# Optimization experiments

Measured on AMD Instinct MI355X. Metric: run time of the kernel, lower is better.

## Reference

```python
import jax, jax.numpy as jnp
import numpy as np

C = 256
CQK = C // 8  # 32

def setup_inputs() -> dict:
    key = jax.random.key(0)
    ks = jax.random.split(key, 9)
    B, H, W = 4, 64, 64
    shp = (B, C, H, W)
    v = jax.random.normal(ks[0], shp, dtype=jnp.float32)
    k = jax.random.normal(ks[1], shp, dtype=jnp.float32)
    q = jax.random.normal(ks[2], shp, dtype=jnp.float32)
    s = 1.0 / np.sqrt(C)
    Wq = jax.random.normal(ks[3], (CQK, C), dtype=jnp.float32) * s
    bq = jnp.zeros((CQK,), dtype=jnp.float32)
    Wk = jax.random.normal(ks[4], (CQK, C), dtype=jnp.float32) * s
    bk = jnp.zeros((CQK,), dtype=jnp.float32)
    Wv = jax.random.normal(ks[5], (C, C), dtype=jnp.float32) * s
    bv = jnp.zeros((C,), dtype=jnp.float32)
    # torch inits gamma=0 (out == v); use small nonzero so attention path is exercised
    gamma = jnp.full((1,), 0.5, dtype=jnp.float32)
    return {"v": v, "k": k, "q": q, "Wq": Wq, "bq": bq, "Wk": Wk, "bk": bk,
            "Wv": Wv, "bv": bv, "gamma": gamma}

def reference(v, k, q, Wq, bq, Wk, bk, Wv, bv, gamma):
    B, Cc, Hh, Ww = v.shape
    N = Hh * Ww
    # 1x1 convs == per-pixel channel matmuls
    pq = jnp.einsum('oc,bchw->bohw', Wq, q) + bq[None, :, None, None]  # B,CQK,H,W
    pk = jnp.einsum('oc,bchw->bohw', Wk, k) + bk[None, :, None, None]
    pv = jnp.einsum('oc,bchw->bohw', Wv, v) + bv[None, :, None, None]  # B,C,H,W
    pq = pq.reshape(B, -1, N)  # B,d,N
    pk = pk.reshape(B, -1, N)
    pv = pv.reshape(B, Cc, N)
    # energy[b,n,m] = <q_n, k_m>; softmax over m (keys)
    energy = jnp.einsum('bdn,bdm->bnm', pq, pk)
    attn = jax.nn.softmax(energy, axis=-1)
    # out[b,c,n] = sum_m v[b,c,m] * attn[b,n,m]
    out = jnp.einsum('bcm,bnm->bcn', pv, attn).reshape(B, Cc, Hh, Ww)
    return gamma * out + v
```

## Files before the change

### kernel.cpp

```cpp
#include <hip/hip_runtime.h>
#include <hip/hip_bf16.h>

typedef __attribute__((ext_vector_type(8))) short short8_t;
typedef __attribute__((ext_vector_type(4))) short short4_t;
typedef __attribute__((ext_vector_type(4))) float float4_t;

#define B_   4
#define C_   256
#define N_   4096
#define DQK  32
#define LOG2E 1.4426950408889634f

#define VMCNT4   asm volatile("s_waitcnt vmcnt(4)" ::: "memory")
#define LGKM0    asm volatile("s_waitcnt lgkmcnt(0)" ::: "memory")
#define SBAR     __builtin_amdgcn_s_barrier()
#define SCHEDB   __builtin_amdgcn_sched_barrier(0)

__device__ __forceinline__ unsigned short f2bf(float x) {
    union { float f; unsigned int u; } v; v.f = x;
    unsigned int r = v.u + 0x7FFFu + ((v.u >> 16) & 1u);
    return (unsigned short)(r >> 16);
}
__device__ __forceinline__ unsigned short f2bf_hw(float x) {
    return __bfloat16_as_ushort(__float2bfloat16(x));
}

__global__ __launch_bounds__(256) void cast_w_k(
        const float* __restrict__ Wq, const float* __restrict__ Wk,
        const float* __restrict__ Wv,
        unsigned short* __restrict__ Wqb, unsigned short* __restrict__ Wkb,
        unsigned short* __restrict__ Wvb) {
    int i = blockIdx.x * 256 + threadIdx.x;
    if (i < 8192)            Wqb[i] = f2bf(Wq[i]);
    else if (i < 16384)      Wkb[i - 8192] = f2bf(Wk[i - 8192]);
    else                     Wvb[i - 16384] = f2bf(Wv[i - 16384]);
}

__global__ __launch_bounds__(256) void proj_qk_k(
        const float* __restrict__ q_in, const float* __restrict__ k_in,
        const unsigned short* __restrict__ Wqb, const unsigned short* __restrict__ Wkb,
        const float* __restrict__ bq, const float* __restrict__ bk,
        unsigned short* __restrict__ pqT, unsigned short* __restrict__ pkT) {
    int b = blockIdx.y, z = blockIdx.z;
    const float* X = z ? k_in : q_in;
    const unsigned short* W = z ? Wkb : Wqb;
    const float* bias = z ? bk : bq;
    unsigned short* P = z ? pkT : pqT;
    float scl = z ? 1.0f : LOG2E;
    int tid = threadIdx.x, wave = tid >> 6, lane = tid & 63, l15 = lane & 15, g = lane >> 4;
    int nb = blockIdx.x * 64 + wave * 16;
    float4_t acc0 = {0.f, 0.f, 0.f, 0.f}, acc1 = {0.f, 0.f, 0.f, 0.f};
    const float* Xcol = X + (size_t)b * C_ * N_ + nb + l15;
#pragma unroll
    for (int kk = 0; kk < 8; ++kk) {
        short8_t a;
#pragma unroll
        for (int j = 0; j < 8; ++j)
            a[j] = (short)f2bf(Xcol[(size_t)(kk * 32 + 8 * g + j) * N_]);
        short8_t b0 = *(const short8_t*)(W + (size_t)l15 * C_ + kk * 32 + 8 * g);
        short8_t b1 = *(const short8_t*)(W + (size_t)(16 + l15) * C_ + kk * 32 + 8 * g);
        acc0 = __builtin_amdgcn_mfma_f32_16x16x32_bf16(a, b0, acc0, 0, 0, 0);
        acc1 = __builtin_amdgcn_mfma_f32_16x16x32_bf16(a, b1, acc1, 0, 0, 0);
    }
#pragma unroll
    for (int r = 0; r < 4; ++r) {
        int n = nb + 4 * g + r;
        P[((size_t)b * N_ + n) * DQK + l15]      = f2bf((acc0[r] + bias[l15]) * scl);
        P[((size_t)b * N_ + n) * DQK + 16 + l15] = f2bf((acc1[r] + bias[16 + l15]) * scl);
    }
}

__global__ __launch_bounds__(256) void proj_v_k(
        const float* __restrict__ v_in, const unsigned short* __restrict__ Wvb,
        const float* __restrict__ bv, unsigned short* __restrict__ pv) {
    int b = blockIdx.y;
    int tid = threadIdx.x, wave = tid >> 6, lane = tid & 63, l15 = lane & 15, g = lane >> 4;
    int mb = blockIdx.x * 16;
    int m = mb + l15;
    int k32 = m & 31;
    int pcol = (k32 < 16) ? ((k32 >> 2) * 8 + (k32 & 3))
                          : (((k32 - 16) >> 2) * 8 + 4 + (k32 & 3));
    int mcol = (m & ~31) + pcol;
    float4_t acc[4];
#pragma unroll
    for (int i = 0; i < 4; ++i) acc[i] = (float4_t){0.f, 0.f, 0.f, 0.f};
    const float* Vcol = v_in + (size_t)b * C_ * N_ + mb + l15;
#pragma unroll
    for (int kk = 0; kk < 8; ++kk) {
        short8_t bf;
#pragma unroll
        for (int j = 0; j < 8; ++j)
            bf[j] = (short)f2bf(Vcol[(size_t)(kk * 32 + 8 * g + j) * N_]);
#pragma unroll
        for (int ct = 0; ct < 4; ++ct) {
            short8_t af = *(const short8_t*)(Wvb + (size_t)(wave * 64 + ct * 16 + l15) * C_ + kk * 32 + 8 * g);
            acc[ct] = __builtin_amdgcn_mfma_f32_16x16x32_bf16(af, bf, acc[ct], 0, 0, 0);
        }
    }
#pragma unroll
    for (int ct = 0; ct < 4; ++ct)
#pragma unroll
        for (int r = 0; r < 4; ++r) {
            int c = wave * 64 + ct * 16 + 4 * g + r;
            pv[((size_t)b * C_ + c) * N_ + mcol] = f2bf(acc[ct][r] + bv[c]);
        }
}

__global__ __launch_bounds__(256, 2) void attn_split_k(
        const unsigned short* __restrict__ pqT, const unsigned short* __restrict__ pkT,
        const unsigned short* __restrict__ pv,
        float* __restrict__ accP, float* __restrict__ lP, int KS) {
    __shared__ __align__(16) unsigned short VT[2][256][64];
    int nqb = gridDim.x;
    int lin = blockIdx.x + nqb * (blockIdx.y + KS * blockIdx.z);
    int cpx = (nqb * KS * 4) >> 3;
    int sl  = (lin & 7) * cpx + (lin >> 3);
    int qbi = sl % nqb;
    int s   = (sl / nqb) % KS;
    int b   = sl / (nqb * KS);

    int kps = N_ / KS, ks0 = s * kps, nt = kps >> 6;
    int tid = threadIdx.x, wave = tid >> 6, lane = tid & 63, l15 = lane & 15, g = lane >> 4;
    int qb = qbi * 64;
    int sw = (l15 & 7) << 4;
    int rl = lane >> 3, cp = lane & 7, cl = cp ^ rl;

    short8_t qf = *(const short8_t*)(pqT + ((size_t)b * N_ + qb + wave * 16 + l15) * DQK + 8 * g);
    float4_t acc[16];
#pragma unroll
    for (int i = 0; i < 16; ++i) acc[i] = (float4_t){0.f, 0.f, 0.f, 0.f};
    float l_acc = 0.f;
    const float4_t zero4 = {0.f, 0.f, 0.f, 0.f};
    const unsigned short* pvb = pv + (size_t)b * C_ * N_;

#define LOADG(dst, base)                                                      \
    _Pragma("unroll")                                                         \
    for (int i_ = 0; i_ < 4; ++i_) {                                          \
        const char* vrow_ = vb + (((base) + i_) * 16 + l15) * 128;            \
        dst[i_][0] = *(const short8_t*)(vrow_ + ((16 * g) ^ sw));             \
        dst[i_][1] = *(const short8_t*)(vrow_ + ((64 + 16 * g) ^ sw));        \
    }
#define MFMAG(frag, ctbase)                                                   \
    _Pragma("unroll")                                                         \
    for (int i_ = 0; i_ < 4; ++i_) {                                          \
        acc[(ctbase) + i_] = __builtin_amdgcn_mfma_f32_16x16x32_bf16(frag[i_][0], pb0, acc[(ctbase) + i_], 0, 0, 0); \
        acc[(ctbase) + i_] = __builtin_amdgcn_mfma_f32_16x16x32_bf16(frag[i_][1], pb1, acc[(ctbase) + i_], 0, 0, 0); \
    }

#pragma unroll
    for (int i = 0; i < 8; ++i) {
        int row0 = wave * 64 + i * 8;
        const unsigned short* src = pvb + (size_t)(row0 + rl) * N_ + ks0 + 8 * cl;
        __builtin_amdgcn_global_load_lds(
            (const __attribute__((address_space(1))) unsigned int*)(const void*)src,
            (__attribute__((address_space(3))) unsigned int*)(void*)&VT[0][row0][0], 16, 0, 0);
    }
    short8_t kfc[4];
#pragma unroll
    for (int it = 0; it < 4; ++it)
        kfc[it] = *(const short8_t*)(pkT + ((size_t)b * N_ + ks0 + 16 * it + l15) * DQK + 8 * g);
    VMCNT4; SCHEDB;
    SBAR;

    for (int t = 0; t < nt; ++t) {
        const int rb = t & 1;
        const int msn = ks0 + (t + 1) * 64;
        if (t + 1 < nt) {
#pragma unroll
            for (int i = 0; i < 8; ++i) {
                int row0 = wave * 64 + i * 8;
                const unsigned short* src = pvb + (size_t)(row0 + rl) * N_ + msn + 8 * cl;
                __builtin_amdgcn_global_load_lds(
                    (const __attribute__((address_space(1))) unsigned int*)(const void*)src,
                    (__attribute__((address_space(3))) unsigned int*)(void*)&VT[rb ^ 1][row0][0], 16, 0, 0);
            }
        }
        SCHEDB;
        const char* vb = (const char*)&VT[rb][0][0];
        short8_t vg0[4][2], vg1[4][2];
        LOADG(vg0, 0);
        LOADG(vg1, 4);
        float4_t sv[4];
#pragma unroll
        for (int it = 0; it < 4; ++it)
            sv[it] = __builtin_amdgcn_mfma_f32_16x16x32_bf16(kfc[it], qf, zero4, 0, 0, 0);
        short8_t kfn[4];
        if (t + 1 < nt) {
#pragma unroll
            for (int it = 0; it < 4; ++it)
                kfn[it] = *(const short8_t*)(pkT + ((size_t)b * N_ + msn + 16 * it + l15) * DQK + 8 * g);
        }
        float p[16];
#pragma unroll
        for (int it = 0; it < 4; ++it)
#pragma unroll
            for (int r = 0; r < 4; ++r)
                p[it * 4 + r] = exp2f(sv[it][r]);
        float s0 = (p[0] + p[1]) + (p[2] + p[3]);
        float s1 = (p[4] + p[5]) + (p[6] + p[7]);
        float s2 = (p[8] + p[9]) + (p[10] + p[11]);
        float s3 = (p[12] + p[13]) + (p[14] + p[15]);
        l_acc += (s0 + s1) + (s2 + s3);
        short8_t pb0, pb1;
#pragma unroll
        for (int j = 0; j < 4; ++j) {
            pb0[j]     = (short)f2bf_hw(p[j]);
            pb0[4 + j] = (short)f2bf_hw(p[4 + j]);
            pb1[j]     = (short)f2bf_hw(p[8 + j]);
            pb1[4 + j] = (short)f2bf_hw(p[12 + j]);
        }
        __builtin_amdgcn_s_setprio(1);
        MFMAG(vg0, 0);
        LOADG(vg0, 8);
        MFMAG(vg1, 4);
        LOADG(vg1, 12);
        MFMAG(vg0, 8);
        MFMAG(vg1, 12);
        __builtin_amdgcn_s_setprio(0);
        if (t + 1 < nt) {
            LGKM0; SCHEDB;
            SBAR;
            VMCNT4; SCHEDB;
            SBAR;
#pragma unroll
            for (int it = 0; it < 4; ++it) kfc[it] = kfn[it];
        }
    }

    l_acc += __shfl_xor(l_acc, 16);
    l_acc += __shfl_xor(l_acc, 32);
    if (g == 0)
        lP[(size_t)(b * KS + s) * N_ + qb + wave * 16 + l15] = l_acc;
    float* accOut = accP + ((size_t)(b * KS + s) * C_) * N_;
#pragma unroll
    for (int ct = 0; ct < 16; ++ct)
#pragma unroll
        for (int r = 0; r < 4; ++r) {
            int c = ct * 16 + 4 * g + r;
            accOut[(size_t)c * N_ + qb + wave * 16 + l15] = acc[ct][r];
        }
#undef LOADG
#undef MFMAG
}

__global__ __launch_bounds__(256) void combine_k(
        const float* __restrict__ accP, const float* __restrict__ lP,
        const float* __restrict__ v_in, const float* __restrict__ gamma,
        float* __restrict__ out, int KS) {
    int i = blockIdx.x * 256 + threadIdx.x;
    const int nq4 = N_ / 4;
    int q0 = (i % nq4) * 4;
    int c  = (i / nq4) % C_;
    int b  = i / (nq4 * C_);
    float4_t num = {0.f, 0.f, 0.f, 0.f}, den = {0.f, 0.f, 0.f, 0.f};
    for (int s = 0; s < KS; ++s) {
        float4_t l4 = *(const float4_t*)(lP + (size_t)(b * KS + s) * N_ + q0);
        float4_t a4 = *(const float4_t*)(accP + ((size_t)(b * KS + s) * C_ + c) * N_ + q0);
#pragma unroll
        for (int j = 0; j < 4; ++j) {
            den[j] += l4[j];
            num[j] += a4[j];
        }
    }
    float gm = gamma[0];
    size_t idx = ((size_t)(b * C_ + c)) * N_ + q0;
    float4_t vi = *(const float4_t*)(v_in + idx);
    float4_t o;
#pragma unroll
    for (int j = 0; j < 4; ++j) o[j] = gm * num[j] / den[j] + vi[j];
    *(float4_t*)(out + idx) = o;
}

extern "C" void kernel_launch(void* const* d_in, const int* in_sizes, int n_in,
                              void* d_out, int out_size, void* d_ws, size_t ws_size,
                              hipStream_t stream) {
    (void)in_sizes; (void)n_in; (void)out_size;
    const float* v_in  = (const float*)d_in[0];
    const float* k_in  = (const float*)d_in[1];
    const float* q_in  = (const float*)d_in[2];
    const float* Wq    = (const float*)d_in[3];
    const float* bq    = (const float*)d_in[4];
    const float* Wk    = (const float*)d_in[5];
    const float* bk    = (const float*)d_in[6];
    const float* Wv    = (const float*)d_in[7];
    const float* bv    = (const float*)d_in[8];
    const float* gamma = (const float*)d_in[9];
    float* out = (float*)d_out;

    char* ws = (char*)d_ws;
    unsigned short* pvb = (unsigned short*)(ws + 0);
    unsigned short* pqT = (unsigned short*)(ws + 8388608);
    unsigned short* pkT = (unsigned short*)(ws + 9437184);
    unsigned short* Wqb = (unsigned short*)(ws + 10485760);
    unsigned short* Wkb = (unsigned short*)(ws + 10502144);
    unsigned short* Wvb = (unsigned short*)(ws + 10518528);
    const size_t base2 = 10649600;

    int KS = 2;
    while (KS > 1) {
        size_t need = base2 + (size_t)KS * 16777216 + (size_t)KS * 262144;
        if (need <= ws_size) break;
        KS >>= 1;
    }
    float* accP = (float*)(ws + base2);
    float* lP   = (float*)(ws + base2 + (size_t)KS * 16777216);

    cast_w_k<<<320, 256, 0, stream>>>(Wq, Wk, Wv, Wqb, Wkb, Wvb);
    proj_qk_k<<<dim3(64, 4, 2), 256, 0, stream>>>(q_in, k_in, Wqb, Wkb, bq, bk, pqT, pkT);
    proj_v_k<<<dim3(256, 4), 256, 0, stream>>>(v_in, Wvb, bv, pvb);
    attn_split_k<<<dim3(64, KS, 4), 256, 0, stream>>>(pqT, pkT, pvb, accP, lP, KS);
    combine_k<<<4096, 256, 0, stream>>>(accP, lP, v_in, gamma, out, KS);
}
```

Baseline: 102.3 us.

## Fuse combine into attention kernel and drop split-K with 8-wave channel split

```diff
diff --git a/kernel.cpp b/kernel.cpp
--- a/kernel.cpp
+++ b/kernel.cpp
@@ -106,37 +106,31 @@
         }
 }
 
-__global__ __launch_bounds__(256, 2) void attn_split_k(
+__global__ __launch_bounds__(512, 2) void attn_fused_k(
         const unsigned short* __restrict__ pqT, const unsigned short* __restrict__ pkT,
-        const unsigned short* __restrict__ pv,
-        float* __restrict__ accP, float* __restrict__ lP, int KS) {
+        const unsigned short* __restrict__ pv, const float* __restrict__ v_in,
+        const float* __restrict__ gamma, float* __restrict__ out) {
     __shared__ __align__(16) unsigned short VT[2][256][64];
-    int nqb = gridDim.x;
-    int lin = blockIdx.x + nqb * (blockIdx.y + KS * blockIdx.z);
-    int cpx = (nqb * KS * 4) >> 3;
-    int sl  = (lin & 7) * cpx + (lin >> 3);
-    int qbi = sl % nqb;
-    int s   = (sl / nqb) % KS;
-    int b   = sl / (nqb * KS);
-
-    int kps = N_ / KS, ks0 = s * kps, nt = kps >> 6;
+    int b = blockIdx.z;
+    int qb = blockIdx.x * 64;
     int tid = threadIdx.x, wave = tid >> 6, lane = tid & 63, l15 = lane & 15, g = lane >> 4;
-    int qb = qbi * 64;
+    int wq = wave & 3, wc = wave >> 2;
     int sw = (l15 & 7) << 4;
     int rl = lane >> 3, cp = lane & 7, cl = cp ^ rl;
-
-    short8_t qf = *(const short8_t*)(pqT + ((size_t)b * N_ + qb + wave * 16 + l15) * DQK + 8 * g);
-    float4_t acc[16];
-#pragma unroll
-    for (int i = 0; i < 16; ++i) acc[i] = (float4_t){0.f, 0.f, 0.f, 0.f};
+    const int nt = N_ / 64;
+
+    short8_t qf = *(const short8_t*)(pqT + ((size_t)b * N_ + qb + wq * 16 + l15) * DQK + 8 * g);
+    float4_t acc[8];
+#pragma unroll
+    for (int i = 0; i < 8; ++i) acc[i] = (float4_t){0.f, 0.f, 0.f, 0.f};
     float l_acc = 0.f;
     const float4_t zero4 = {0.f, 0.f, 0.f, 0.f};
     const unsigned short* pvb = pv + (size_t)b * C_ * N_;
 
-#define LOADG(dst, base)                                                      \
+#define LOADG(dst, ctbase)                                                    \
     _Pragma("unroll")                                                         \
     for (int i_ = 0; i_ < 4; ++i_) {                                          \
-        const char* vrow_ = vb + (((base) + i_) * 16 + l15) * 128;            \
+        const char* vrow_ = vb + (((ctbase) + i_) * 16 + l15) * 128;          \
         dst[i_][0] = *(const short8_t*)(vrow_ + ((16 * g) ^ sw));             \
         dst[i_][1] = *(const short8_t*)(vrow_ + ((64 + 16 * g) ^ sw));        \
     }
@@ -148,9 +142,9 @@
     }
 
 #pragma unroll
-    for (int i = 0; i < 8; ++i) {
-        int row0 = wave * 64 + i * 8;
-        const unsigned short* src = pvb + (size_t)(row0 + rl) * N_ + ks0 + 8 * cl;
+    for (int i = 0; i < 4; ++i) {
+        int row0 = i * 64 + wave * 8;
+        const unsigned short* src = pvb + (size_t)(row0 + rl) * N_ + 8 * cl;
         __builtin_amdgcn_global_load_lds(
             (const __attribute__((address_space(1))) unsigned int*)(const void*)src,
             (__attribute__((address_space(3))) unsigned int*)(void*)&VT[0][row0][0], 16, 0, 0);
@@ -158,17 +152,17 @@
     short8_t kfc[4];
 #pragma unroll
     for (int it = 0; it < 4; ++it)
-        kfc[it] = *(const short8_t*)(pkT + ((size_t)b * N_ + ks0 + 16 * it + l15) * DQK + 8 * g);
+        kfc[it] = *(const short8_t*)(pkT + ((size_t)b * N_ + 16 * it + l15) * DQK + 8 * g);
     VMCNT4; SCHEDB;
     SBAR;
 
     for (int t = 0; t < nt; ++t) {
         const int rb = t & 1;
-        const int msn = ks0 + (t + 1) * 64;
+        const int msn = (t + 1) * 64;
         if (t + 1 < nt) {
 #pragma unroll
-            for (int i = 0; i < 8; ++i) {
-                int row0 = wave * 64 + i * 8;
+            for (int i = 0; i < 4; ++i) {
+                int row0 = i * 64 + wave * 8;
                 const unsigned short* src = pvb + (size_t)(row0 + rl) * N_ + msn + 8 * cl;
                 __builtin_amdgcn_global_load_lds(
                     (const __attribute__((address_space(1))) unsigned int*)(const void*)src,
@@ -176,7 +170,7 @@
             }
         }
         SCHEDB;
-        const char* vb = (const char*)&VT[rb][0][0];
+        const char* vb = (const char*)&VT[rb][0][0] + wc * 16384;
         short8_t vg0[4][2], vg1[4][2];
         LOADG(vg0, 0);
         LOADG(vg1, 4);
@@ -211,11 +205,7 @@
         }
         __builtin_amdgcn_s_setprio(1);
         MFMAG(vg0, 0);
-        LOADG(vg0, 8);
         MFMAG(vg1, 4);
-        LOADG(vg1, 12);
-        MFMAG(vg0, 8);
-        MFMAG(vg1, 12);
         __builtin_amdgcn_s_setprio(0);
         if (t + 1 < nt) {
             LGKM0; SCHEDB;
@@ -229,52 +219,24 @@
 
     l_acc += __shfl_xor(l_acc, 16);
     l_acc += __shfl_xor(l_acc, 32);
-    if (g == 0)
-        lP[(size_t)(b * KS + s) * N_ + qb + wave * 16 + l15] = l_acc;
-    float* accOut = accP + ((size_t)(b * KS + s) * C_) * N_;
-#pragma unroll
-    for (int ct = 0; ct < 16; ++ct)
+    float inv = 1.f / l_acc;
+    float gm = gamma[0];
+#pragma unroll
+    for (int ct = 0; ct < 8; ++ct)
 #pragma unroll
         for (int r = 0; r < 4; ++r) {
-            int c = ct * 16 + 4 * g + r;
-            accOut[(size_t)c * N_ + qb + wave * 16 + l15] = acc[ct][r];
+            int c = wc * 128 + ct * 16 + 4 * g + r;
+            size_t idx = ((size_t)(b * C_ + c)) * N_ + qb + wq * 16 + l15;
+            out[idx] = gm * acc[ct][r] * inv + v_in[idx];
         }
 #undef LOADG
 #undef MFMAG
-}
-
-__global__ __launch_bounds__(256) void combine_k(
-        const float* __restrict__ accP, const float* __restrict__ lP,
-        const float* __restrict__ v_in, const float* __restrict__ gamma,
-        float* __restrict__ out, int KS) {
-    int i = blockIdx.x * 256 + threadIdx.x;
-    const int nq4 = N_ / 4;
-    int q0 = (i % nq4) * 4;
-    int c  = (i / nq4) % C_;
-    int b  = i / (nq4 * C_);
-    float4_t num = {0.f, 0.f, 0.f, 0.f}, den = {0.f, 0.f, 0.f, 0.f};
-    for (int s = 0; s < KS; ++s) {
-        float4_t l4 = *(const float4_t*)(lP + (size_t)(b * KS + s) * N_ + q0);
-        float4_t a4 = *(const float4_t*)(accP + ((size_t)(b * KS + s) * C_ + c) * N_ + q0);
-#pragma unroll
-        for (int j = 0; j < 4; ++j) {
-            den[j] += l4[j];
-            num[j] += a4[j];
-        }
-    }
-    float gm = gamma[0];
-    size_t idx = ((size_t)(b * C_ + c)) * N_ + q0;
-    float4_t vi = *(const float4_t*)(v_in + idx);
-    float4_t o;
-#pragma unroll
-    for (int j = 0; j < 4; ++j) o[j] = gm * num[j] / den[j] + vi[j];
-    *(float4_t*)(out + idx) = o;
 }
 
 extern "C" void kernel_launch(void* const* d_in, const int* in_sizes, int n_in,
                               void* d_out, int out_size, void* d_ws, size_t ws_size,
                               hipStream_t stream) {
-    (void)in_sizes; (void)n_in; (void)out_size;
+    (void)in_sizes; (void)n_in; (void)out_size; (void)ws_size;
     const float* v_in  = (const float*)d_in[0];
     const float* k_in  = (const float*)d_in[1];
     const float* q_in  = (const float*)d_in[2];
@@ -294,20 +256,9 @@
     unsigned short* Wqb = (unsigned short*)(ws + 10485760);
     unsigned short* Wkb = (unsigned short*)(ws + 10502144);
     unsigned short* Wvb = (unsigned short*)(ws + 10518528);
-    const size_t base2 = 10649600;
-
-    int KS = 2;
-    while (KS > 1) {
-        size_t need = base2 + (size_t)KS * 16777216 + (size_t)KS * 262144;
-        if (need <= ws_size) break;
-        KS >>= 1;
-    }
-    float* accP = (float*)(ws + base2);
-    float* lP   = (float*)(ws + base2 + (size_t)KS * 16777216);
 
     cast_w_k<<<320, 256, 0, stream>>>(Wq, Wk, Wv, Wqb, Wkb, Wvb);
     proj_qk_k<<<dim3(64, 4, 2), 256, 0, stream>>>(q_in, k_in, Wqb, Wkb, bq, bk, pqT, pkT);
     proj_v_k<<<dim3(256, 4), 256, 0, stream>>>(v_in, Wvb, bv, pvb);
-    attn_split_k<<<dim3(64, KS, 4), 256, 0, stream>>>(pqT, pkT, pvb, accP, lP, KS);
-    combine_k<<<4096, 256, 0, stream>>>(accP, lP, v_in, gamma, out, KS);
-}
+    attn_fused_k<<<dim3(64, 1, 4), 512, 0, stream>>>(pqT, pkT, pvb, v_in, gamma, out);
+}
```

Result: slower. 123.1 us (+20.3%).

## Retile split-K attention waves into 2x2 query/channel grid with MFMA row sums

Applied to the files above, without the earlier changes.

```diff
diff --git a/kernel.cpp b/kernel.cpp
--- a/kernel.cpp
+++ b/kernel.cpp
@@ -121,31 +121,28 @@
 
     int kps = N_ / KS, ks0 = s * kps, nt = kps >> 6;
     int tid = threadIdx.x, wave = tid >> 6, lane = tid & 63, l15 = lane & 15, g = lane >> 4;
+    int wq = wave & 1, wc = wave >> 1;
     int qb = qbi * 64;
     int sw = (l15 & 7) << 4;
     int rl = lane >> 3, cp = lane & 7, cl = cp ^ rl;
 
-    short8_t qf = *(const short8_t*)(pqT + ((size_t)b * N_ + qb + wave * 16 + l15) * DQK + 8 * g);
-    float4_t acc[16];
-#pragma unroll
-    for (int i = 0; i < 16; ++i) acc[i] = (float4_t){0.f, 0.f, 0.f, 0.f};
-    float l_acc = 0.f;
+    short8_t qf[2];
+#pragma unroll
+    for (int qs = 0; qs < 2; ++qs)
+        qf[qs] = *(const short8_t*)(pqT + ((size_t)b * N_ + qb + wq * 32 + qs * 16 + l15) * DQK + 8 * g);
+    float4_t acc[2][8];
+#pragma unroll
+    for (int qs = 0; qs < 2; ++qs)
+#pragma unroll
+        for (int i = 0; i < 8; ++i) acc[qs][i] = (float4_t){0.f, 0.f, 0.f, 0.f};
+    float4_t accl[2];
+    accl[0] = (float4_t){0.f, 0.f, 0.f, 0.f};
+    accl[1] = (float4_t){0.f, 0.f, 0.f, 0.f};
+    short8_t onef;
+#pragma unroll
+    for (int j = 0; j < 8; ++j) onef[j] = (short)0x3F80;
     const float4_t zero4 = {0.f, 0.f, 0.f, 0.f};
     const unsigned short* pvb = pv + (size_t)b * C_ * N_;
-
-#define LOADG(dst, base)                                                      \
-    _Pragma("unroll")                                                         \
-    for (int i_ = 0; i_ < 4; ++i_) {                                          \
-        const char* vrow_ = vb + (((base) + i_) * 16 + l15) * 128;            \
-        dst[i_][0] = *(const short8_t*)(vrow_ + ((16 * g) ^ sw));             \
-        dst[i_][1] = *(const short8_t*)(vrow_ + ((64 + 16 * g) ^ sw));        \
-    }
-#define MFMAG(frag, ctbase)                                                   \
-    _Pragma("unroll")                                                         \
-    for (int i_ = 0; i_ < 4; ++i_) {                                          \
-        acc[(ctbase) + i_] = __builtin_amdgcn_mfma_f32_16x16x32_bf16(frag[i_][0], pb0, acc[(ctbase) + i_], 0, 0, 0); \
-        acc[(ctbase) + i_] = __builtin_amdgcn_mfma_f32_16x16x32_bf16(frag[i_][1], pb1, acc[(ctbase) + i_], 0, 0, 0); \
-    }
 
 #pragma unroll
     for (int i = 0; i < 8; ++i) {
@@ -176,46 +173,51 @@
             }
         }
         SCHEDB;
-        const char* vb = (const char*)&VT[rb][0][0];
-        short8_t vg0[4][2], vg1[4][2];
-        LOADG(vg0, 0);
-        LOADG(vg1, 4);
-        float4_t sv[4];
-#pragma unroll
-        for (int it = 0; it < 4; ++it)
-            sv[it] = __builtin_amdgcn_mfma_f32_16x16x32_bf16(kfc[it], qf, zero4, 0, 0, 0);
+        float4_t sv[2][4];
+#pragma unroll
+        for (int qs = 0; qs < 2; ++qs)
+#pragma unroll
+            for (int it = 0; it < 4; ++it)
+                sv[qs][it] = __builtin_amdgcn_mfma_f32_16x16x32_bf16(kfc[it], qf[qs], zero4, 0, 0, 0);
         short8_t kfn[4];
         if (t + 1 < nt) {
 #pragma unroll
             for (int it = 0; it < 4; ++it)
                 kfn[it] = *(const short8_t*)(pkT + ((size_t)b * N_ + msn + 16 * it + l15) * DQK + 8 * g);
         }
-        float p[16];
-#pragma unroll
-        for (int it = 0; it < 4; ++it)
-#pragma unroll
-            for (int r = 0; r < 4; ++r)
-                p[it * 4 + r] = exp2f(sv[it][r]);
-        float s0 = (p[0] + p[1]) + (p[2] + p[3]);
-        float s1 = (p[4] + p[5]) + (p[6] + p[7]);
-        float s2 = (p[8] + p[9]) + (p[10] + p[11]);
-        float s3 = (p[12] + p[13]) + (p[14] + p[15]);
-        l_acc += (s0 + s1) + (s2 + s3);
-        short8_t pb0, pb1;
-#pragma unroll
-        for (int j = 0; j < 4; ++j) {
-            pb0[j]     = (short)f2bf_hw(p[j]);
-            pb0[4 + j] = (short)f2bf_hw(p[4 + j]);
-            pb1[j]     = (short)f2bf_hw(p[8 + j]);
-            pb1[4 + j] = (short)f2bf_hw(p[12 + j]);
-        }
+        short8_t pb[2][2];
+#pragma unroll
+        for (int qs = 0; qs < 2; ++qs) {
+            float p[16];
+#pragma unroll
+            for (int it = 0; it < 4; ++it)
+#pragma unroll
+                for (int r = 0; r < 4; ++r)
+                    p[it * 4 + r] = exp2f(sv[qs][it][r]);
+#pragma unroll
+            for (int j = 0; j < 4; ++j) {
+                pb[qs][0][j]     = (short)f2bf_hw(p[j]);
+                pb[qs][0][4 + j] = (short)f2bf_hw(p[4 + j]);
+                pb[qs][1][j]     = (short)f2bf_hw(p[8 + j]);
+                pb[qs][1][4 + j] = (short)f2bf_hw(p[12 + j]);
+            }
+        }
+        const char* vb = (const char*)&VT[rb][0][0] + wc * 16384;
         __builtin_amdgcn_s_setprio(1);
-        MFMAG(vg0, 0);
-        LOADG(vg0, 8);
-        MFMAG(vg1, 4);
-        LOADG(vg1, 12);
-        MFMAG(vg0, 8);
-        MFMAG(vg1, 12);
+#pragma unroll
+        for (int ct = 0; ct < 8; ++ct) {
+            const char* vrow = vb + (ct * 16 + l15) * 128;
+            short8_t va0 = *(const short8_t*)(vrow + ((16 * g) ^ sw));
+            short8_t va1 = *(const short8_t*)(vrow + ((64 + 16 * g) ^ sw));
+            acc[0][ct] = __builtin_amdgcn_mfma_f32_16x16x32_bf16(va0, pb[0][0], acc[0][ct], 0, 0, 0);
+            acc[0][ct] = __builtin_amdgcn_mfma_f32_16x16x32_bf16(va1, pb[0][1], acc[0][ct], 0, 0, 0);
+            acc[1][ct] = __builtin_amdgcn_mfma_f32_16x16x32_bf16(va0, pb[1][0], acc[1][ct], 0, 0, 0);
+            acc[1][ct] = __builtin_amdgcn_mfma_f32_16x16x32_bf16(va1, pb[1][1], acc[1][ct], 0, 0, 0);
+        }
+        accl[0] = __builtin_amdgcn_mfma_f32_16x16x32_bf16(onef, pb[0][0], accl[0], 0, 0, 0);
+        accl[0] = __builtin_amdgcn_mfma_f32_16x16x32_bf16(onef, pb[0][1], accl[0], 0, 0, 0);
+        accl[1] = __builtin_amdgcn_mfma_f32_16x16x32_bf16(onef, pb[1][0], accl[1], 0, 0, 0);
+        accl[1] = __builtin_amdgcn_mfma_f32_16x16x32_bf16(onef, pb[1][1], accl[1], 0, 0, 0);
         __builtin_amdgcn_s_setprio(0);
         if (t + 1 < nt) {
             LGKM0; SCHEDB;
@@ -227,20 +229,20 @@
         }
     }
 
-    l_acc += __shfl_xor(l_acc, 16);
-    l_acc += __shfl_xor(l_acc, 32);
-    if (g == 0)
-        lP[(size_t)(b * KS + s) * N_ + qb + wave * 16 + l15] = l_acc;
     float* accOut = accP + ((size_t)(b * KS + s) * C_) * N_;
 #pragma unroll
-    for (int ct = 0; ct < 16; ++ct)
-#pragma unroll
-        for (int r = 0; r < 4; ++r) {
-            int c = ct * 16 + 4 * g + r;
-            accOut[(size_t)c * N_ + qb + wave * 16 + l15] = acc[ct][r];
-        }
-#undef LOADG
-#undef MFMAG
+    for (int qs = 0; qs < 2; ++qs) {
+        int q = qb + wq * 32 + qs * 16 + l15;
+#pragma unroll
+        for (int ct = 0; ct < 8; ++ct)
+#pragma unroll
+            for (int r = 0; r < 4; ++r) {
+                int c = wc * 128 + ct * 16 + 4 * g + r;
+                accOut[(size_t)c * N_ + q] = acc[qs][ct][r];
+            }
+        if (wc == 0 && g == 0)
+            lP[(size_t)(b * KS + s) * N_ + q] = accl[qs][0];
+    }
 }
 
 __global__ __launch_bounds__(256) void combine_k(
```

After: 112.3 us. +9.7%, slower.

## Software-pipeline QK/exp one tile ahead and compute row sums via MFMA

Applied to the files above, without the earlier changes.

```diff
diff --git a/kernel.cpp b/kernel.cpp
--- a/kernel.cpp
+++ b/kernel.cpp
@@ -12,6 +12,7 @@
 #define LOG2E 1.4426950408889634f
 
 #define VMCNT4   asm volatile("s_waitcnt vmcnt(4)" ::: "memory")
+#define VMCNT0   asm volatile("s_waitcnt vmcnt(0)" ::: "memory")
 #define LGKM0    asm volatile("s_waitcnt lgkmcnt(0)" ::: "memory")
 #define SBAR     __builtin_amdgcn_s_barrier()
 #define SCHEDB   __builtin_amdgcn_sched_barrier(0)
@@ -123,114 +124,107 @@
     int tid = threadIdx.x, wave = tid >> 6, lane = tid & 63, l15 = lane & 15, g = lane >> 4;
     int qb = qbi * 64;
     int sw = (l15 & 7) << 4;
-    int rl = lane >> 3, cp = lane & 7, cl = cp ^ rl;
+    int rl = lane >> 3, cl = (lane & 7) ^ rl;
 
     short8_t qf = *(const short8_t*)(pqT + ((size_t)b * N_ + qb + wave * 16 + l15) * DQK + 8 * g);
     float4_t acc[16];
 #pragma unroll
     for (int i = 0; i < 16; ++i) acc[i] = (float4_t){0.f, 0.f, 0.f, 0.f};
-    float l_acc = 0.f;
+    float4_t accl = {0.f, 0.f, 0.f, 0.f};
+    short8_t onef;
+#pragma unroll
+    for (int j = 0; j < 8; ++j) onef[j] = (short)0x3F80;
     const float4_t zero4 = {0.f, 0.f, 0.f, 0.f};
     const unsigned short* pvb = pv + (size_t)b * C_ * N_;
-
-#define LOADG(dst, base)                                                      \
+    const char* pkTb = (const char*)pkT + (size_t)b * N_ * DQK * 2;
+
+    unsigned soff[8];
+#pragma unroll
+    for (int i = 0; i < 8; ++i)
+        soff[i] = (unsigned)(((wave * 64 + i * 8 + rl) * N_ + ks0 + 8 * cl) * 2);
+    unsigned koff = (unsigned)(((ks0 + l15) * DQK + 8 * g) * 2);
+    int off1 = (16 * g) ^ sw, off2 = (64 + 16 * g) ^ sw;
+    const char* vbA = (const char*)&VT[0][0][0] + l15 * 128 + off1;
+    const char* vbB = (const char*)&VT[0][0][0] + l15 * 128 + off2;
+
+#define STAGE(RBUF)                                                           \
     _Pragma("unroll")                                                         \
-    for (int i_ = 0; i_ < 4; ++i_) {                                          \
-        const char* vrow_ = vb + (((base) + i_) * 16 + l15) * 128;            \
-        dst[i_][0] = *(const short8_t*)(vrow_ + ((16 * g) ^ sw));             \
-        dst[i_][1] = *(const short8_t*)(vrow_ + ((64 + 16 * g) ^ sw));        \
-    }
-#define MFMAG(frag, ctbase)                                                   \
+    for (int i_ = 0; i_ < 8; ++i_) {                                          \
+        __builtin_amdgcn_global_load_lds(                                     \
+            (const __attribute__((address_space(1))) unsigned int*)(const void*)((const char*)pvb + soff[i_]), \
+            (__attribute__((address_space(3))) unsigned int*)(void*)&VT[RBUF][wave * 64 + i_ * 8][0], 16, 0, 0); \
+    }                                                                          \
     _Pragma("unroll")                                                         \
-    for (int i_ = 0; i_ < 4; ++i_) {                                          \
-        acc[(ctbase) + i_] = __builtin_amdgcn_mfma_f32_16x16x32_bf16(frag[i_][0], pb0, acc[(ctbase) + i_], 0, 0, 0); \
-        acc[(ctbase) + i_] = __builtin_amdgcn_mfma_f32_16x16x32_bf16(frag[i_][1], pb1, acc[(ctbase) + i_], 0, 0, 0); \
-    }
-
-#pragma unroll
-    for (int i = 0; i < 8; ++i) {
-        int row0 = wave * 64 + i * 8;
-        const unsigned short* src = pvb + (size_t)(row0 + rl) * N_ + ks0 + 8 * cl;
-        __builtin_amdgcn_global_load_lds(
-            (const __attribute__((address_space(1))) unsigned int*)(const void*)src,
-            (__attribute__((address_space(3))) unsigned int*)(void*)&VT[0][row0][0], 16, 0, 0);
-    }
-    short8_t kfc[4];
-#pragma unroll
-    for (int it = 0; it < 4; ++it)
-        kfc[it] = *(const short8_t*)(pkT + ((size_t)b * N_ + ks0 + 16 * it + l15) * DQK + 8 * g);
-    VMCNT4; SCHEDB;
+    for (int i_ = 0; i_ < 8; ++i_) soff[i_] += 128;
+
+#define KFLOAD(DST)                                                           \
+    _Pragma("unroll")                                                         \
+    for (int it_ = 0; it_ < 4; ++it_)                                         \
+        DST[it_] = *(const short8_t*)(pkTb + koff + it_ * 1024);              \
+    koff += 4096;
+
+#define QKEXP(KF, PN0, PN1)                                                   \
+    {                                                                          \
+        float4_t sv_[4];                                                       \
+        _Pragma("unroll")                                                      \
+        for (int it_ = 0; it_ < 4; ++it_)                                      \
+            sv_[it_] = __builtin_amdgcn_mfma_f32_16x16x32_bf16(KF[it_], qf, zero4, 0, 0, 0); \
+        float p_[16];                                                          \
+        _Pragma("unroll")                                                      \
+        for (int it_ = 0; it_ < 4; ++it_)                                      \
+            _Pragma("unroll")                                                  \
+            for (int r_ = 0; r_ < 4; ++r_)                                     \
+                p_[it_ * 4 + r_] = exp2f(sv_[it_][r_]);                        \
+        _Pragma("unroll")                                                      \
+        for (int j_ = 0; j_ < 4; ++j_) {                                       \
+            PN0[j_]     = (short)f2bf_hw(p_[j_]);                              \
+            PN0[4 + j_] = (short)f2bf_hw(p_[4 + j_]);                          \
+            PN1[j_]     = (short)f2bf_hw(p_[8 + j_]);                          \
+            PN1[4 + j_] = (short)f2bf_hw(p_[12 + j_]);                         \
+        }                                                                      \
+    }
+
+#define PVPH(RB, PC0, PC1)                                                    \
+    __builtin_amdgcn_s_setprio(1);                                            \
+    _Pragma("unroll")                                                         \
+    for (int ct_ = 0; ct_ < 16; ++ct_) {                                      \
+        short8_t va0_ = *(const short8_t*)(vbA + (RB) * 32768 + ct_ * 2048);  \
+        short8_t va1_ = *(const short8_t*)(vbB + (RB) * 32768 + ct_ * 2048);  \
+        acc[ct_] = __builtin_amdgcn_mfma_f32_16x16x32_bf16(va0_, PC0, acc[ct_], 0, 0, 0); \
+        acc[ct_] = __builtin_amdgcn_mfma_f32_16x16x32_bf16(va1_, PC1, acc[ct_], 0, 0, 0); \
+    }                                                                          \
+    accl = __builtin_amdgcn_mfma_f32_16x16x32_bf16(onef, PC0, accl, 0, 0, 0); \
+    accl = __builtin_amdgcn_mfma_f32_16x16x32_bf16(onef, PC1, accl, 0, 0, 0); \
+    __builtin_amdgcn_s_setprio(0);
+
+#define BODY(RB, KFC, KFN, PC0, PC1, PN0, PN1, TT)                            \
+    if ((TT) + 1 < nt) { STAGE(RB ^ 1) }                                      \
+    SCHEDB;                                                                   \
+    KFLOAD(KFN)                                                               \
+    QKEXP(KFC, PN0, PN1)                                                      \
+    PVPH(RB, PC0, PC1)                                                        \
+    LGKM0; SCHEDB;                                                            \
+    SBAR;                                                                     \
+    VMCNT4; SCHEDB;                                                           \
     SBAR;
 
-    for (int t = 0; t < nt; ++t) {
-        const int rb = t & 1;
-        const int msn = ks0 + (t + 1) * 64;
-        if (t + 1 < nt) {
-#pragma unroll
-            for (int i = 0; i < 8; ++i) {
-                int row0 = wave * 64 + i * 8;
-                const unsigned short* src = pvb + (size_t)(row0 + rl) * N_ + msn + 8 * cl;
-                __builtin_amdgcn_global_load_lds(
-                    (const __attribute__((address_space(1))) unsigned int*)(const void*)src,
-                    (__attribute__((address_space(3))) unsigned int*)(void*)&VT[rb ^ 1][row0][0], 16, 0, 0);
-            }
-        }
-        SCHEDB;
-        const char* vb = (const char*)&VT[rb][0][0];
-        short8_t vg0[4][2], vg1[4][2];
-        LOADG(vg0, 0);
-        LOADG(vg1, 4);
-        float4_t sv[4];
-#pragma unroll
-        for (int it = 0; it < 4; ++it)
-            sv[it] = __builtin_amdgcn_mfma_f32_16x16x32_bf16(kfc[it], qf, zero4, 0, 0, 0);
-        short8_t kfn[4];
-        if (t + 1 < nt) {
-#pragma unroll
-            for (int it = 0; it < 4; ++it)
-                kfn[it] = *(const short8_t*)(pkT + ((size_t)b * N_ + msn + 16 * it + l15) * DQK + 8 * g);
-        }
-        float p[16];
-#pragma unroll
-        for (int it = 0; it < 4; ++it)
-#pragma unroll
-            for (int r = 0; r < 4; ++r)
-                p[it * 4 + r] = exp2f(sv[it][r]);
-        float s0 = (p[0] + p[1]) + (p[2] + p[3]);
-        float s1 = (p[4] + p[5]) + (p[6] + p[7]);
-        float s2 = (p[8] + p[9]) + (p[10] + p[11]);
-        float s3 = (p[12] + p[13]) + (p[14] + p[15]);
-        l_acc += (s0 + s1) + (s2 + s3);
-        short8_t pb0, pb1;
-#pragma unroll
-        for (int j = 0; j < 4; ++j) {
-            pb0[j]     = (short)f2bf_hw(p[j]);
-            pb0[4 + j] = (short)f2bf_hw(p[4 + j]);
-            pb1[j]     = (short)f2bf_hw(p[8 + j]);
-            pb1[4 + j] = (short)f2bf_hw(p[12 + j]);
-        }
-        __builtin_amdgcn_s_setprio(1);
-        MFMAG(vg0, 0);
-        LOADG(vg0, 8);
-        MFMAG(vg1, 4);
-        LOADG(vg1, 12);
-        MFMAG(vg0, 8);
-        MFMAG(vg1, 12);
-        __builtin_amdgcn_s_setprio(0);
-        if (t + 1 < nt) {
-            LGKM0; SCHEDB;
-            SBAR;
-            VMCNT4; SCHEDB;
-            SBAR;
-#pragma unroll
-            for (int it = 0; it < 4; ++it) kfc[it] = kfn[it];
-        }
-    }
-
-    l_acc += __shfl_xor(l_acc, 16);
-    l_acc += __shfl_xor(l_acc, 32);
+    short8_t kfA[4], kfB[4];
+    short8_t pbA0, pbA1, pbB0, pbB1;
+    STAGE(0)
+    SCHEDB;
+    KFLOAD(kfB)
+    KFLOAD(kfA)
+    VMCNT0; SCHEDB;
+    QKEXP(kfB, pbB0, pbB1)
+    SBAR;
+
+    for (int t = 0; t < nt; t += 2) {
+        BODY(0, kfA, kfB, pbB0, pbB1, pbA0, pbA1, t)
+        BODY(1, kfB, kfA, pbA0, pbA1, pbB0, pbB1, t + 1)
+    }
+
     if (g == 0)
-        lP[(size_t)(b * KS + s) * N_ + qb + wave * 16 + l15] = l_acc;
+        lP[(size_t)(b * KS + s) * N_ + qb + wave * 16 + l15] = accl[0];
     float* accOut = accP + ((size_t)(b * KS + s) * C_) * N_;
 #pragma unroll
     for (int ct = 0; ct < 16; ++ct)
@@ -239,8 +233,11 @@
             int c = ct * 16 + 4 * g + r;
             accOut[(size_t)c * N_ + qb + wave * 16 + l15] = acc[ct][r];
         }
-#undef LOADG
-#undef MFMAG
+#undef STAGE
+#undef KFLOAD
+#undef QKEXP
+#undef PVPH
+#undef BODY
 }
 
 __global__ __launch_bounds__(256) void combine_k(
@@ -291,10 +288,10 @@
     unsigned short* pvb = (unsigned short*)(ws + 0);
     unsigned short* pqT = (unsigned short*)(ws + 8388608);
     unsigned short* pkT = (unsigned short*)(ws + 9437184);
-    unsigned short* Wqb = (unsigned short*)(ws + 10485760);
-    unsigned short* Wkb = (unsigned short*)(ws + 10502144);
-    unsigned short* Wvb = (unsigned short*)(ws + 10518528);
-    const size_t base2 = 10649600;
+    unsigned short* Wqb = (unsigned short*)(ws + 10502144);
+    unsigned short* Wkb = (unsigned short*)(ws + 10518528);
+    unsigned short* Wvb = (unsigned short*)(ws + 10534912);
+    const size_t base2 = 10665984;
 
     int KS = 2;
     while (KS > 1) {
```

New measurement: 101.4 us. No clear change (-0.9%).
